# Performance work log

Measured on AMD Instinct MI355X. Metric: run time of the kernel, lower is better.

## Reference

```python
import jax, jax.numpy as jnp
import numpy as np

# Dimensions: state [N, d, n, 2] with last axis = (q, p)
N, D, NN = 256, 8, 32
FEAT = D * NN          # flattened q features = 256
HID = 256              # MLP hidden width
DT = 0.01              # integration step
STEPS = 100            # number of RK4 steps (sequential)


def setup_inputs() -> dict:
    key = jax.random.key(0)
    k0, k1, k2 = jax.random.split(key, 3)
    x0 = 0.1 * jax.random.normal(k0, (N, D, NN, 2), dtype=jnp.float32)
    W1 = jax.random.normal(k1, (FEAT, HID), dtype=jnp.float32) / np.float32(np.sqrt(FEAT))
    b1 = jnp.zeros((HID,), dtype=jnp.float32)
    W2 = jax.random.normal(k2, (HID, 1), dtype=jnp.float32) / np.float32(np.sqrt(HID))
    b2 = jnp.zeros((1,), dtype=jnp.float32)
    return {"x0": x0, "W1": W1, "b1": b1, "W2": W2, "b2": b2}


def _hamiltonian(x, W1, b1, W2, b2):
    # x: [N, d, n, 2] -> H: [N]
    q = x[..., 0]
    p = x[..., 1]
    kinetic = 0.5 * jnp.sum(p * p, axis=(1, 2))          # [N]
    qf = q.reshape(q.shape[0], -1)                        # [N, d*n]
    h = jnp.tanh(qf @ W1 + b1)                            # [N, HID]
    V = (h @ W2 + b2)[:, 0]                               # [N]
    return kinetic + V


def _vector_field(x, params):
    # Hamiltonian vector field: dq/dt = dH/dp, dp/dt = -dH/dq (t-independent)
    g = jax.grad(lambda xx: jnp.sum(_hamiltonian(xx, *params)))(x)  # [N,d,n,2]
    return jnp.stack([g[..., 1], -g[..., 0]], axis=-1)


def _rk4_step(x, eps, params):
    k1 = _vector_field(x, params)
    k2 = _vector_field(x + 0.5 * eps * k1, params)
    k3 = _vector_field(x + 0.5 * eps * k2, params)
    k4 = _vector_field(x + eps * k3, params)
    return x + (eps / 6.0) * (k1 + 2.0 * k2 + 2.0 * k3 + k4)


def reference(x0, W1, b1, W2, b2):
    params = (W1, b1, W2, b2)
    eps = jnp.float32(DT)

    def step(x, _):
        return _rk4_step(x, eps, params), None

    xT, _ = jax.lax.scan(step, x0, None, length=STEPS)
    return xT
```

## Files before the change

### kernel.cpp

```cpp
#include <hip/hip_runtime.h>
#include <stdint.h>


typedef _Float16 v8h __attribute__((ext_vector_type(8)));
typedef float v4f __attribute__((ext_vector_type(4)));

#define NSTEPS 100
#define NEX 25
#define WS 264
#define US 272

#define MFMA_AV(C, A, B) \
    asm("v_mfma_f32_16x16x32_f16 %0, %1, %2, %0" : "+v"(C) : "v"(A), "a"(B))

__device__ __forceinline__ float bfly4(float x) {
    float a = x, b = x;
    asm("v_permlane16_swap_b32 %0, %1" : "+v"(a), "+v"(b));
    float s = a + b;
    float c = s, d = s;
    asm("v_permlane32_swap_b32 %0, %1" : "+v"(c), "+v"(d));
    return c + d;
}

__device__ __forceinline__ float ueval2(float zz, float w4) {
    float e_ = __expf(zz);
    float r_ = __builtin_amdgcn_rcpf(e_ + 1.f);
    return w4 * __builtin_fmaf(-r_, r_, r_);
}

__global__ __launch_bounds__(1024, 4)
void ham_kernel(const float* __restrict__ x0, const float* __restrict__ W1,
                const float* __restrict__ b1, const float* __restrict__ W2,
                float* __restrict__ out)
{
    __shared__ __align__(16)  _Float16 wldsT[256 * WS];
    __shared__ __align__(128) char     upool[20480];
    float*    mscr = (float*)upool;
    _Float16* ubuf = (_Float16*)upool;

    const int t = threadIdx.x;
    const int w = t >> 6;
    const int l = t & 63;
    const int quad = l >> 4;
    const int s = l & 15;
    const int c0 = 16 * w + s;
    const int blk = blockIdx.x;
    const int sel = (s & 3) * US;

    {
        const int c = t & 255;
        const int rbase = (t >> 8) * 64;
        #pragma unroll 1
        for (int r0 = 0; r0 < 64; r0 += 8) {
            v8h h;
            #pragma unroll
            for (int j = 0; j < 8; ++j)
                h[j] = (_Float16)W1[(rbase + r0 + j) * 256 + c];
            *(v8h*)(wldsT + c * WS + rbase + r0) = h;
        }
    }
    __syncthreads();

    v8h wF0[8];
    #pragma unroll
    for (int kk = 0; kk < 8; ++kk)
        wF0[kk] = *(const v8h*)(wldsT + c0 * WS + 32 * kk + 8 * quad);

    v8h wM0[8];
    float* scr0 = mscr + w * 320;
    #pragma unroll
    for (int kb = 0; kb < 16; ++kb) {
        v8h aM[8];
        #pragma unroll
        for (int kk = 0; kk < 8; ++kk)
            aM[kk] = *(const v8h*)(wldsT + (16 * kb + s) * WS
                                          + 32 * kk + 8 * quad);
        v4f D0 = {0.f,0.f,0.f,0.f};
        #pragma unroll
        for (int kk = 0; kk < 8; ++kk)
            D0 = __builtin_amdgcn_mfma_f32_16x16x32_f16(aM[kk], wF0[kk], D0, 0, 0, 0);
        *(v4f*)(scr0 + s * 20 + 4 * quad) = D0;
        asm volatile("s_waitcnt lgkmcnt(0)" ::: "memory");
        if ((quad >> 1) == (kb & 1)) {
            #pragma unroll
            for (int j = 0; j < 8; ++j)
                wM0[kb >> 1][j] = (_Float16)scr0[s * 20 + 8 * (quad & 1) + j];
        }
        asm volatile("s_waitcnt lgkmcnt(0)" ::: "memory");
    }
    __syncthreads();

    const float b1r0 = b1[c0];
    const float w4 = 4.f * W2[c0];
    float2 qp0 = ((const float2*)(x0 + (size_t)blk * 512))[c0];
    const float q0o0 = qp0.x, p0o0 = qp0.y;

    if (quad == 0) {
        ubuf[c0] = (_Float16)q0o0;
        ubuf[US + c0] = (_Float16)p0o0;
        ubuf[2 * US + c0] = (_Float16)0.f;
        ubuf[3 * US + c0] = (_Float16)0.f;
    }
    __syncthreads();
    float z1, P;
    {
        const _Float16* ab = ubuf + sel + 8 * quad;
        v4f C0a = {0.f,0.f,0.f,0.f}, C0b = {0.f,0.f,0.f,0.f};
        #pragma unroll
        for (int kk = 0; kk < 8; kk += 2) {
            v8h a0 = *(const v8h*)(ab + 32 * kk);
            v8h a1 = *(const v8h*)(ab + 32 * (kk + 1));
            C0a = __builtin_amdgcn_mfma_f32_16x16x32_f16(a0, wF0[kk], C0a, 0, 0, 0);
            C0b = __builtin_amdgcn_mfma_f32_16x16x32_f16(a1, wF0[kk + 1], C0b, 0, 0, 0);
        }
        v4f C0s = C0a + C0b;
        z1 = C0s[0] + b1r0;  P = C0s[1];
    }
    __syncthreads();

    const float dt = 0.01f, hdt = 0.005f, dt6 = 0.01f / 6.f;
    const float dtdt6 = dt * dt6, hdt2 = hdt * hdt, dthdt = dt * hdt;
    const float fourdt = 4.f * dt;
    const float qf  = (float)quad;
    const float cPn   = -(qf * 0.25f * dt6);
    const float K2cz1 = 2.f * qf * dt;
    const float K2B   = qf * (4.f - qf) * dtdt6 * 0.25f;
    const float K2Vn  = -(qf * dtdt6 * 0.5f);
    const float K2hdt = 2.f * hdt;
    const float K2hdt2n = -2.f * hdt2;
    const float K2dt  = 2.f * dt;
    const float K2dthdtn = -2.f * dthdt;
    const float wB  = 3.f - qf;

    const int c0w = c0 ^ (quad << 3);
    _Float16* wbase0 = ubuf + 4 * quad * US + c0w;
    const int sx = (s >> 2) & 3;
    const _Float16* rb = ubuf + s * US + 8 * (quad ^ sx);

    float SBp = 0.f, SVp = 0.f;
    float Y1L = 0.f, Y2L = 0.f;
    float S1p = 0.f, S23p = 0.f;
    float cn = 99.f - qf;

    #pragma unroll 1
    for (int e = 0; e < NEX; ++e) {
        const int bo = (e & 1) * (16 * US);

        float Pp  = __builtin_fmaf(cPn, SBp, P);
        float zp2 = __builtin_fmaf(K2cz1, P, z1 + z1);
        zp2 = __builtin_fmaf(K2B, SBp, zp2);
        zp2 = __builtin_fmaf(K2Vn, SVp, zp2);
        float zb2 = __builtin_fmaf(K2hdt, Pp, zp2);
        float zc2 = __builtin_fmaf(K2hdt2n, Y1L, zb2);
        float zd2 = __builtin_fmaf(K2dt, Pp, zp2);
        zd2 = __builtin_fmaf(K2dthdtn, Y2L, zd2);

        float ua = ueval2(zp2, w4);
        float ub = ueval2(zb2, w4);
        float uc = ueval2(zc2, w4);
        float ud = ueval2(zd2, w4);

        _Float16* wp0 = wbase0 + bo;
        wp0[0]      = (_Float16)ua;
        wp0[US]     = (_Float16)ub;
        wp0[2 * US] = (_Float16)uc;
        wp0[3 * US] = (_Float16)ud;
        __syncthreads();

        v4f C0s;
        {
            const _Float16* ab = rb + bo;
            v4f C0a = {0.f,0.f,0.f,0.f}, C0b = {0.f,0.f,0.f,0.f};
            #pragma unroll
            for (int kk = 0; kk < 8; kk += 2) {
                v8h a0 = *(const v8h*)(ab + 32 * kk);
                v8h a1 = *(const v8h*)(ab + 32 * (kk + 1));
                MFMA_AV(C0a, a0, wM0[kk]);
                MFMA_AV(C0b, a1, wM0[kk + 1]);
            }
            C0s = C0a + C0b;
        }

        float Y1 = C0s[0], Y2 = C0s[1], Y3 = C0s[2], Y4 = C0s[3];
        float tA = Y2 + Y3;
        float A  = Y1 + tA;
        float B  = A + tA + Y4;
        float V  = __builtin_fmaf(wB, B, A);
        float SB = bfly4(B);
        float SV = bfly4(V);

        z1 = __builtin_fmaf(fourdt, P, z1);
        z1 = __builtin_fmaf(-dtdt6, SV, z1);
        P  = __builtin_fmaf(-dt6, SB, P);

        SBp = SB;  SVp = SV;  Y1L = Y1;  Y2L = Y2;

        float tv = ub + uc;
        float sp = __builtin_fmaf(2.f, tv, ua + ud);
        float sq = ua + tv;
        S1p += sp;
        S23p = __builtin_fmaf(cn, sp, S23p) + sq;
        cn -= 4.f;
    }

    const float S1f  = bfly4(S1p);
    const float S23f = bfly4(S23p);
    __syncthreads();
    if (quad == 0) {
        ubuf[c0] = (_Float16)S1f;
        ubuf[US + c0] = (_Float16)S23f;
        ubuf[2 * US + c0] = (_Float16)0.f;
        ubuf[3 * US + c0] = (_Float16)0.f;
    }
    __syncthreads();
    v8h wBt0[8];
    #pragma unroll
    for (int kk = 0; kk < 8; ++kk)
        #pragma unroll
        for (int j = 0; j < 8; ++j)
            wBt0[kk][j] = wldsT[(32 * kk + 8 * quad + j) * WS + c0];
    float D10, D20;
    {
        const _Float16* ab = ubuf + sel + 8 * quad;
        v4f C0a = {0.f,0.f,0.f,0.f}, C0b = {0.f,0.f,0.f,0.f};
        #pragma unroll
        for (int kk = 0; kk < 8; kk += 2) {
            v8h a0 = *(const v8h*)(ab + 32 * kk);
            v8h a1 = *(const v8h*)(ab + 32 * (kk + 1));
            C0a = __builtin_amdgcn_mfma_f32_16x16x32_f16(a0, wBt0[kk], C0a, 0, 0, 0);
            C0b = __builtin_amdgcn_mfma_f32_16x16x32_f16(a1, wBt0[kk + 1], C0b, 0, 0, 0);
        }
        v4f C0s = C0a + C0b;
        D10 = C0s[0];  D20 = C0s[1];
    }
    const float dt6e = 0.01f / 6.f, dtdt6e = 0.01f * dt6e;
    float pT0 = p0o0 - dt6e * D10;
    float qT0 = q0o0 + 0.01f * (float)NSTEPS * p0o0 - dtdt6e * D20;

    if (quad == 0)
        ((float2*)(out + (size_t)blk * 512))[c0] = make_float2(qT0, pT0);
}

extern "C" void kernel_launch(void* const* d_in, const int* in_sizes, int n_in,
                              void* d_out, int out_size, void* d_ws, size_t ws_size,
                              hipStream_t stream) {
    const float* x0 = (const float*)d_in[0];
    const float* W1 = (const float*)d_in[1];
    const float* b1 = (const float*)d_in[2];
    const float* W2 = (const float*)d_in[3];
    float* out = (float*)d_out;
    hipLaunchKernelGGL(ham_kernel, dim3(256), dim3(1024), 0, stream,
                       x0, W1, b1, W2, out);
}
```

Measured before the change: 97.78 us.

## Process eight RK4 steps per barrier with XOR-swizzled LDS layout

Each loop iteration now handles two groups of four RK4 steps (8 rows), so the 100 steps take 12 full iterations plus a 4-step tail instead of 25 iterations. This halves the number of block-wide barriers and LDS round trips, and issues two independent MFMA chains per iteration to overlap latency. The LDS layout replaces row padding with an XOR swizzle, which frees space to reuse the weight buffer as the update buffer, and the transposed-weight fragment load moves before the main loop. In exchange there is more register pressure, more complex coefficient bookkeeping, and possible numeric drift from the restructured step extrapolation.

Result: slower. 113.1 us (+15.6%).

```diff
diff --git a/kernel.cpp b/kernel.cpp
--- a/kernel.cpp
+++ b/kernel.cpp
@@ -5,10 +5,7 @@
 typedef _Float16 v8h __attribute__((ext_vector_type(8)));
 typedef float v4f __attribute__((ext_vector_type(4)));
 
-#define NSTEPS 100
-#define NEX 25
-#define WS 264
-#define US 272
+#define NFULL 12
 
 #define MFMA_AV(C, A, B) \
     asm("v_mfma_f32_16x16x32_f16 %0, %1, %2, %0" : "+v"(C) : "v"(A), "a"(B))
@@ -33,10 +30,9 @@
                 const float* __restrict__ b1, const float* __restrict__ W2,
                 float* __restrict__ out)
 {
-    __shared__ __align__(16)  _Float16 wldsT[256 * WS];
-    __shared__ __align__(128) char     upool[20480];
-    float*    mscr = (float*)upool;
-    _Float16* ubuf = (_Float16*)upool;
+    __shared__ __align__(128) _Float16 wldsT[256 * 256];
+    __shared__ __align__(16)  float    mscr[16 * 320];
+    _Float16* ubuf = wldsT;
 
     const int t = threadIdx.x;
     const int w = t >> 6;
@@ -45,36 +41,39 @@
     const int s = l & 15;
     const int c0 = 16 * w + s;
     const int blk = blockIdx.x;
-    const int sel = (s & 3) * US;
+    const int kq = 8 * quad;
 
     {
         const int c = t & 255;
         const int rbase = (t >> 8) * 64;
+        const int csw = (c & 7) << 3;
         #pragma unroll 1
         for (int r0 = 0; r0 < 64; r0 += 8) {
             v8h h;
             #pragma unroll
             for (int j = 0; j < 8; ++j)
                 h[j] = (_Float16)W1[(rbase + r0 + j) * 256 + c];
-            *(v8h*)(wldsT + c * WS + rbase + r0) = h;
+            *(v8h*)(wldsT + c * 256 + ((rbase + r0) ^ csw)) = h;
         }
     }
     __syncthreads();
 
     v8h wF0[8];
+    const int c0sw = (c0 & 7) << 3;
     #pragma unroll
     for (int kk = 0; kk < 8; ++kk)
-        wF0[kk] = *(const v8h*)(wldsT + c0 * WS + 32 * kk + 8 * quad);
+        wF0[kk] = *(const v8h*)(wldsT + c0 * 256 + ((32 * kk + kq) ^ c0sw));
 
     v8h wM0[8];
     float* scr0 = mscr + w * 320;
+    const int ssw = (s & 7) << 3;
     #pragma unroll
     for (int kb = 0; kb < 16; ++kb) {
         v8h aM[8];
         #pragma unroll
         for (int kk = 0; kk < 8; ++kk)
-            aM[kk] = *(const v8h*)(wldsT + (16 * kb + s) * WS
-                                          + 32 * kk + 8 * quad);
+            aM[kk] = *(const v8h*)(wldsT + (16 * kb + s) * 256
+                                          + ((32 * kk + kq) ^ ssw));
         v4f D0 = {0.f,0.f,0.f,0.f};
         #pragma unroll
         for (int kk = 0; kk < 8; ++kk)
@@ -88,6 +87,13 @@
         }
         asm volatile("s_waitcnt lgkmcnt(0)" ::: "memory");
     }
+
+    v8h wBt0[8];
+    #pragma unroll
+    for (int kk = 0; kk < 8; ++kk)
+        #pragma unroll
+        for (int j = 0; j < 8; ++j)
+            wBt0[kk][j] = wldsT[(32 * kk + kq + j) * 256 + (c0 ^ (j << 3))];
     __syncthreads();
 
     const float b1r0 = b1[c0];
@@ -96,15 +102,16 @@
     const float q0o0 = qp0.x, p0o0 = qp0.y;
 
     if (quad == 0) {
-        ubuf[c0] = (_Float16)q0o0;
-        ubuf[US + c0] = (_Float16)p0o0;
-        ubuf[2 * US + c0] = (_Float16)0.f;
-        ubuf[3 * US + c0] = (_Float16)0.f;
+        ubuf[0 * 256 + (c0 ^ 0)]  = (_Float16)q0o0;
+        ubuf[1 * 256 + (c0 ^ 8)]  = (_Float16)p0o0;
+        ubuf[2 * 256 + (c0 ^ 16)] = (_Float16)0.f;
+        ubuf[3 * 256 + (c0 ^ 24)] = (_Float16)0.f;
     }
     __syncthreads();
     float z1, P;
     {
-        const _Float16* ab = ubuf + sel + 8 * quad;
+        const int rowp = s & 3;
+        const _Float16* ab = ubuf + rowp * 256 + 8 * (quad ^ rowp);
         v4f C0a = {0.f,0.f,0.f,0.f}, C0b = {0.f,0.f,0.f,0.f};
         #pragma unroll
         for (int kk = 0; kk < 8; kk += 2) {
@@ -120,108 +127,168 @@
 
     const float dt = 0.01f, hdt = 0.005f, dt6 = 0.01f / 6.f;
     const float dtdt6 = dt * dt6, hdt2 = hdt * hdt, dthdt = dt * hdt;
-    const float fourdt = 4.f * dt;
-    const float qf  = (float)quad;
-    const float cPn   = -(qf * 0.25f * dt6);
-    const float K2cz1 = 2.f * qf * dt;
-    const float K2B   = qf * (4.f - qf) * dtdt6 * 0.25f;
-    const float K2Vn  = -(qf * dtdt6 * 0.5f);
-    const float K2hdt = 2.f * hdt;
-    const float K2hdt2n = -2.f * hdt2;
-    const float K2dt  = 2.f * dt;
-    const float K2dthdtn = -2.f * dthdt;
-    const float wB  = 3.f - qf;
-
-    const int c0w = c0 ^ (quad << 3);
-    _Float16* wbase0 = ubuf + 4 * quad * US + c0w;
-    const int sx = (s >> 2) & 3;
-    const _Float16* rb = ubuf + s * US + 8 * (quad ^ sx);
+    const float K8dt = 8.f * dt, K4dt = 4.f * dt;
+    const float qf1 = (float)quad, qf2 = qf1 + 4.f;
+    const float cPn1 = -(qf1 * 0.125f * dt6), cPn2 = -(qf2 * 0.125f * dt6);
+    const float Kz1a = 2.f * qf1 * dt,        Kz1b = 2.f * qf2 * dt;
+    const float KB1 = dtdt6 * qf1 * (8.f - qf1) * 0.125f;
+    const float KB2 = dtdt6 * qf2 * (8.f - qf2) * 0.125f;
+    const float KVn1 = -(qf1 * dtdt6 * 0.25f), KVn2 = -(qf2 * dtdt6 * 0.25f);
+    const float K2hdt = 2.f * hdt, K2hdt2n = -2.f * hdt2;
+    const float K2dt = 2.f * dt,   K2dthdtn = -2.f * dthdt;
+    const float w3q = 3.f - qf1;
+
+    const int swhi = (s & 4) << 3;
+    const int pbase = s * 256 + (kq ^ ((s & 3) << 3));
+    const int beven = pbase + swhi;
+    const int bodd  = pbase - swhi;
+    const int R0 = 4 * quad;
+    const int wo0 = (R0 + 0) * 256 + (c0 ^ (((R0 + 0) & 7) << 3));
+    const int wo1 = (R0 + 1) * 256 + (c0 ^ (((R0 + 1) & 7) << 3));
+    const int wo2 = (R0 + 2) * 256 + (c0 ^ (((R0 + 2) & 7) << 3));
+    const int wo3 = (R0 + 3) * 256 + (c0 ^ (((R0 + 3) & 7) << 3));
 
     float SBp = 0.f, SVp = 0.f;
-    float Y1L = 0.f, Y2L = 0.f;
+    float Y1L1 = 0.f, Y2L1 = 0.f, Y1L2 = 0.f, Y2L2 = 0.f;
     float S1p = 0.f, S23p = 0.f;
-    float cn = 99.f - qf;
+    float cn = 99.f - qf1;
 
     #pragma unroll 1
-    for (int e = 0; e < NEX; ++e) {
-        const int bo = (e & 1) * (16 * US);
-
-        float Pp  = __builtin_fmaf(cPn, SBp, P);
-        float zp2 = __builtin_fmaf(K2cz1, P, z1 + z1);
-        zp2 = __builtin_fmaf(K2B, SBp, zp2);
-        zp2 = __builtin_fmaf(K2Vn, SVp, zp2);
-        float zb2 = __builtin_fmaf(K2hdt, Pp, zp2);
-        float zc2 = __builtin_fmaf(K2hdt2n, Y1L, zb2);
-        float zd2 = __builtin_fmaf(K2dt, Pp, zp2);
-        zd2 = __builtin_fmaf(K2dthdtn, Y2L, zd2);
-
-        float ua = ueval2(zp2, w4);
-        float ub = ueval2(zb2, w4);
-        float uc = ueval2(zc2, w4);
-        float ud = ueval2(zd2, w4);
-
-        _Float16* wp0 = wbase0 + bo;
-        wp0[0]      = (_Float16)ua;
-        wp0[US]     = (_Float16)ub;
-        wp0[2 * US] = (_Float16)uc;
-        wp0[3 * US] = (_Float16)ud;
+    for (int e = 0; e < NFULL; ++e) {
+        const int bo = (e & 1) << 13;
+
+        float z1d = z1 + z1;
+        float Pp1 = __builtin_fmaf(cPn1, SBp, P);
+        float zp21 = __builtin_fmaf(Kz1a, P, z1d);
+        zp21 = __builtin_fmaf(KB1, SBp, zp21);
+        zp21 = __builtin_fmaf(KVn1, SVp, zp21);
+        float zb21 = __builtin_fmaf(K2hdt, Pp1, zp21);
+        float zc21 = __builtin_fmaf(K2hdt2n, Y1L1, zb21);
+        float zd21 = __builtin_fmaf(K2dt, Pp1, zp21);
+        zd21 = __builtin_fmaf(K2dthdtn, Y2L1, zd21);
+        float Pp2 = __builtin_fmaf(cPn2, SBp, P);
+        float zp22 = __builtin_fmaf(Kz1b, P, z1d);
+        zp22 = __builtin_fmaf(KB2, SBp, zp22);
+        zp22 = __builtin_fmaf(KVn2, SVp, zp22);
+        float zb22 = __builtin_fmaf(K2hdt, Pp2, zp22);
+        float zc22 = __builtin_fmaf(K2hdt2n, Y1L2, zb22);
+        float zd22 = __builtin_fmaf(K2dt, Pp2, zp22);
+        zd22 = __builtin_fmaf(K2dthdtn, Y2L2, zd22);
+
+        float ua1 = ueval2(zp21, w4), ub1 = ueval2(zb21, w4);
+        float uc1 = ueval2(zc21, w4), ud1 = ueval2(zd21, w4);
+        float ua2 = ueval2(zp22, w4), ub2 = ueval2(zb22, w4);
+        float uc2 = ueval2(zc22, w4), ud2 = ueval2(zd22, w4);
+
+        ubuf[bo + wo0] = (_Float16)ua1;  ubuf[bo + wo0 + 4096] = (_Float16)ua2;
+        ubuf[bo + wo1] = (_Float16)ub1;  ubuf[bo + wo1 + 4096] = (_Float16)ub2;
+        ubuf[bo + wo2] = (_Float16)uc1;  ubuf[bo + wo2 + 4096] = (_Float16)uc2;
+        ubuf[bo + wo3] = (_Float16)ud1;  ubuf[bo + wo3 + 4096] = (_Float16)ud2;
         __syncthreads();
 
-        v4f C0s;
+        v4f C0a = {0.f,0.f,0.f,0.f}, C0b = {0.f,0.f,0.f,0.f};
+        v4f C1a = {0.f,0.f,0.f,0.f}, C1b = {0.f,0.f,0.f,0.f};
         {
-            const _Float16* ab = rb + bo;
-            v4f C0a = {0.f,0.f,0.f,0.f}, C0b = {0.f,0.f,0.f,0.f};
+            const _Float16* pe = ubuf + bo + beven;
+            const _Float16* po = ubuf + bo + bodd;
             #pragma unroll
             for (int kk = 0; kk < 8; kk += 2) {
-                v8h a0 = *(const v8h*)(ab + 32 * kk);
-                v8h a1 = *(const v8h*)(ab + 32 * (kk + 1));
-                MFMA_AV(C0a, a0, wM0[kk]);
-                MFMA_AV(C0b, a1, wM0[kk + 1]);
+                v8h a00 = *(const v8h*)(pe + 32 * kk);
+                v8h a01 = *(const v8h*)(po + 32 * (kk + 1));
+                v8h a10 = *(const v8h*)(pe + 32 * kk + 4096);
+                v8h a11 = *(const v8h*)(po + 32 * (kk + 1) + 4096);
+                MFMA_AV(C0a, a00, wM0[kk]);
+                MFMA_AV(C1a, a10, wM0[kk]);
+                MFMA_AV(C0b, a01, wM0[kk + 1]);
+                MFMA_AV(C1b, a11, wM0[kk + 1]);
             }
-            C0s = C0a + C0b;
-        }
-
-        float Y1 = C0s[0], Y2 = C0s[1], Y3 = C0s[2], Y4 = C0s[3];
-        float tA = Y2 + Y3;
-        float A  = Y1 + tA;
-        float B  = A + tA + Y4;
-        float V  = __builtin_fmaf(wB, B, A);
-        float SB = bfly4(B);
+        }
+
+        v4f C0 = C0a + C0b, C1 = C1a + C1b;
+        float Y11 = C0[0], Y21 = C0[1], Y31 = C0[2], Y41 = C0[3];
+        float Y12 = C1[0], Y22 = C1[1], Y32 = C1[2], Y42 = C1[3];
+        float tA1 = Y21 + Y31, A1 = Y11 + tA1, B1 = A1 + tA1 + Y41;
+        float tA2 = Y22 + Y32, A2 = Y12 + tA2, B2 = A2 + tA2 + Y42;
+        float Bs = B1 + B2;
+        float V = __builtin_fmaf(w3q, Bs, A1 + A2);
+        V = __builtin_fmaf(4.f, B1, V);
+        float SB = bfly4(Bs);
         float SV = bfly4(V);
 
-        z1 = __builtin_fmaf(fourdt, P, z1);
+        z1 = __builtin_fmaf(K8dt, P, z1);
         z1 = __builtin_fmaf(-dtdt6, SV, z1);
         P  = __builtin_fmaf(-dt6, SB, P);
 
-        SBp = SB;  SVp = SV;  Y1L = Y1;  Y2L = Y2;
-
-        float tv = ub + uc;
-        float sp = __builtin_fmaf(2.f, tv, ua + ud);
-        float sq = ua + tv;
-        S1p += sp;
-        S23p = __builtin_fmaf(cn, sp, S23p) + sq;
-        cn -= 4.f;
+        SBp = SB;  SVp = SV;
+        Y1L1 = Y11; Y2L1 = Y21; Y1L2 = Y12; Y2L2 = Y22;
+
+        float tv1 = ub1 + uc1, sp1 = __builtin_fmaf(2.f, tv1, ua1 + ud1);
+        float sq1 = ua1 + tv1;
+        float tv2 = ub2 + uc2, sp2 = __builtin_fmaf(2.f, tv2, ua2 + ud2);
+        float sq2 = ua2 + tv2;
+        S1p += sp1 + sp2;
+        S23p = __builtin_fmaf(cn, sp1, S23p) + sq1;
+        S23p = __builtin_fmaf(cn - 4.f, sp2, S23p) + sq2;
+        cn -= 8.f;
+    }
+
+    {
+        float z1d = z1 + z1;
+        float Pp1 = __builtin_fmaf(cPn1, SBp, P);
+        float zp21 = __builtin_fmaf(Kz1a, P, z1d);
+        zp21 = __builtin_fmaf(KB1, SBp, zp21);
+        zp21 = __builtin_fmaf(KVn1, SVp, zp21);
+        float zb21 = __builtin_fmaf(K2hdt, Pp1, zp21);
+        float zc21 = __builtin_fmaf(K2hdt2n, Y1L1, zb21);
+        float zd21 = __builtin_fmaf(K2dt, Pp1, zp21);
+        zd21 = __builtin_fmaf(K2dthdtn, Y2L1, zd21);
+        float ua1 = ueval2(zp21, w4), ub1 = ueval2(zb21, w4);
+        float uc1 = ueval2(zc21, w4), ud1 = ueval2(zd21, w4);
+        ubuf[wo0] = (_Float16)ua1;  ubuf[wo1] = (_Float16)ub1;
+        ubuf[wo2] = (_Float16)uc1;  ubuf[wo3] = (_Float16)ud1;
+        __syncthreads();
+
+        v4f C0a = {0.f,0.f,0.f,0.f}, C0b = {0.f,0.f,0.f,0.f};
+        {
+            const _Float16* pe = ubuf + beven;
+            const _Float16* po = ubuf + bodd;
+            #pragma unroll
+            for (int kk = 0; kk < 8; kk += 2) {
+                v8h a00 = *(const v8h*)(pe + 32 * kk);
+                v8h a01 = *(const v8h*)(po + 32 * (kk + 1));
+                MFMA_AV(C0a, a00, wM0[kk]);
+                MFMA_AV(C0b, a01, wM0[kk + 1]);
+            }
+        }
+        v4f C0 = C0a + C0b;
+        float Y11 = C0[0], Y21 = C0[1], Y31 = C0[2], Y41 = C0[3];
+        float tA1 = Y21 + Y31, A1 = Y11 + tA1, B1 = A1 + tA1 + Y41;
+        float V = __builtin_fmaf(w3q, B1, A1);
+        float SB = bfly4(B1);
+        float SV = bfly4(V);
+        z1 = __builtin_fmaf(K4dt, P, z1);
+        z1 = __builtin_fmaf(-dtdt6, SV, z1);
+        P  = __builtin_fmaf(-dt6, SB, P);
+        float tv1 = ub1 + uc1, sp1 = __builtin_fmaf(2.f, tv1, ua1 + ud1);
+        float sq1 = ua1 + tv1;
+        S1p += sp1;
+        S23p = __builtin_fmaf(cn, sp1, S23p) + sq1;
     }
 
     const float S1f  = bfly4(S1p);
     const float S23f = bfly4(S23p);
     __syncthreads();
     if (quad == 0) {
-        ubuf[c0] = (_Float16)S1f;
-        ubuf[US + c0] = (_Float16)S23f;
-        ubuf[2 * US + c0] = (_Float16)0.f;
-        ubuf[3 * US + c0] = (_Float16)0.f;
-    }
-    __syncthreads();
-    v8h wBt0[8];
-    #pragma unroll
-    for (int kk = 0; kk < 8; ++kk)
-        #pragma unroll
-        for (int j = 0; j < 8; ++j)
-            wBt0[kk][j] = wldsT[(32 * kk + 8 * quad + j) * WS + c0];
+        ubuf[0 * 256 + (c0 ^ 0)]  = (_Float16)S1f;
+        ubuf[1 * 256 + (c0 ^ 8)]  = (_Float16)S23f;
+        ubuf[2 * 256 + (c0 ^ 16)] = (_Float16)0.f;
+        ubuf[3 * 256 + (c0 ^ 24)] = (_Float16)0.f;
+    }
+    __syncthreads();
     float D10, D20;
     {
-        const _Float16* ab = ubuf + sel + 8 * quad;
+        const int rowp = s & 3;
+        const _Float16* ab = ubuf + rowp * 256 + 8 * (quad ^ rowp);
         v4f C0a = {0.f,0.f,0.f,0.f}, C0b = {0.f,0.f,0.f,0.f};
         #pragma unroll
         for (int kk = 0; kk < 8; kk += 2) {
@@ -235,7 +302,7 @@
     }
     const float dt6e = 0.01f / 6.f, dtdt6e = 0.01f * dt6e;
     float pT0 = p0o0 - dt6e * D10;
-    float qT0 = q0o0 + 0.01f * (float)NSTEPS * p0o0 - dtdt6e * D20;
+    float qT0 = q0o0 + 0.01f * 100.f * p0o0 - dtdt6e * D20;
 
     if (quad == 0)
         ((float2*)(out + (size_t)blk * 512))[c0] = make_float2(qT0, pT0);
```
